# Kernel optimization log

Hardware: AMD Instinct MI355X
Metric: run time of the kernel (lower is better)

The kernel has to match this reference:

```python
import jax, jax.numpy as jnp
import numpy as np

B, F, V, E, D1, DD, L2 = 4096, 32, 50000, 64, 256, 16, 128


def setup_inputs() -> dict:
    key = jax.random.key(0)
    ks = jax.random.split(key, 16)
    s = 0.05  # small init scale to keep tanh unsaturated
    return {
        "sparse": jax.random.randint(ks[0], (B, F), 0, V, dtype=jnp.int32),
        "dense": jax.random.normal(ks[1], (B, DD), dtype=jnp.float32),
        "tables": jax.random.normal(ks[2], (F, V, E), dtype=jnp.float32) * s,
        "Wz": jax.random.normal(ks[3], (D1, F, E), dtype=jnp.float32) * s,
        "bz": jnp.zeros((D1,), jnp.float32),
        "Wpi": jax.random.normal(ks[4], (D1, F, F), dtype=jnp.float32) * s,
        "bpi": jnp.zeros((D1,), jnp.float32),
        "Wpo": jax.random.normal(ks[5], (D1, E, E), dtype=jnp.float32) * s,
        "bpo": jnp.zeros((D1,), jnp.float32),
        "B1": jax.random.normal(ks[6], (D1,), dtype=jnp.float32) * s,
        "W1": jax.random.normal(ks[7], (D1 + DD, D1), dtype=jnp.float32) * s,
        "b1": jnp.zeros((D1,), jnp.float32),
        "W2": jax.random.normal(ks[8], (D1, L2), dtype=jnp.float32) * s,
        "b2": jnp.zeros((L2,), jnp.float32),
        "W3": jax.random.normal(ks[9], (L2, 1), dtype=jnp.float32) * s,
        "b3": jnp.zeros((1,), jnp.float32),
    }


def reference(sparse, dense, tables, Wz, bz, Wpi, bpi, Wpo, bpo, B1,
              W1, b1, W2, b2, W3, b3):
    # Embedding lookup: per-field table gather -> [B, F, E]
    emb = tables[jnp.arange(F)[None, :], sparse]
    # Lz: Conv1d(in=F, kernel=E) over [B, F, E] == full contraction -> [B, D1]
    Lz = jnp.einsum('bfe,dfe->bd', emb, Wz) + bz
    # Inner product: [B, F, F], then Conv1d(in=F, kernel=F) full contraction
    inner = jnp.einsum('bie,bje->bij', emb, emb)
    Lp_inner = jnp.einsum('bij,dij->bd', inner, Wpi) + bpi
    # Outer product: sum_{i,j} x_i^T x_j == s^T s with s = sum_i x_i (exact rewrite)
    s = emb.sum(axis=1)                      # [B, E]
    outer = s[:, :, None] * s[:, None, :]    # [B, E, E]
    Lp_outer = jnp.einsum('bij,dij->bd', outer, Wpo) + bpo
    L1 = Lz + Lp_inner + Lp_outer + B1       # [B, D1]
    deep_x = jnp.concatenate([L1, dense], axis=1)  # [B, D1+DD]
    h = jnp.tanh(deep_x @ W1 + b1)
    h = jnp.tanh(h @ W2 + b2)
    out = (h @ W3 + b3)[:, 0]                # [B]
    return out
```

## Files before the change

kernel.cpp:

```cpp
#include <hip/hip_runtime.h>
#include <hip/hip_bf16.h>

#define B_    4096
#define F_    32
#define V_    50000
#define E_    64
#define D1_   256
#define DD_   16
#define L2N_  128
#define KX    3072
#define KTOT  7168
#define NKC   8

typedef __bf16 bf16x8 __attribute__((ext_vector_type(8)));
typedef float  f32x4  __attribute__((ext_vector_type(4)));

typedef __attribute__((address_space(1))) const void gvoid;
typedef __attribute__((address_space(3))) void svoid;

__device__ __forceinline__ ushort f2b(float f){
  __bf16 h = (__bf16)f; return __builtin_bit_cast(ushort, h);
}
__device__ __forceinline__ float b2f(ushort u){
  return __uint_as_float(((uint)u) << 16);
}
__device__ __forceinline__ float blo(uint u){ return __uint_as_float(u << 16); }
__device__ __forceinline__ float bhi(uint u){ return __uint_as_float(u & 0xffff0000u); }
__device__ __forceinline__ void gload16(const void* g, void* l){
  __builtin_amdgcn_global_load_lds((gvoid*)g, (svoid*)l, 16, 0, 0);
}

__global__ __launch_bounds__(256) void prep_gather(
    const float* __restrict__ Wz, const float* __restrict__ Wpi,
    const float* __restrict__ Wpo, const float* __restrict__ W1,
    const float* __restrict__ W2,
    const int* __restrict__ sparse, const float* __restrict__ tables,
    ushort* __restrict__ WBb, ushort* __restrict__ W1b, ushort* __restrict__ W2b,
    ushort* __restrict__ Xb, ushort* __restrict__ Sb) {
  __shared__ ushort gsh[4][32 * 72];
  int bid = blockIdx.x, t = threadIdx.x;
  if (bid < 640) {
    if (bid < 256) {
      int n = bid;
#pragma unroll
      for (int j = 0; j < 7; ++j) {
        int k4 = (j * 256 + t) * 4;
        float4 v;
        if (k4 < 2048)      v = *(const float4*)&Wz [(size_t)n * 2048 + k4];
        else if (k4 < 3072) v = *(const float4*)&Wpi[(size_t)n * 1024 + (k4 - 2048)];
        else                v = *(const float4*)&Wpo[(size_t)n * 4096 + (k4 - 3072)];
        ushort4 o = make_ushort4(f2b(v.x), f2b(v.y), f2b(v.z), f2b(v.w));
        *(ushort4*)&WBb[(size_t)n * KTOT + k4] = o;
      }
    } else if (bid < 512) {
      int n = bid - 256;
      float v0 = (t < 272) ? W1[(size_t)t * 256 + n] : 0.f;
      W1b[(size_t)n * 288 + t] = f2b(v0);
      if (t < 32) {
        int k2 = 256 + t;
        float v1 = (k2 < 272) ? W1[(size_t)k2 * 256 + n] : 0.f;
        W1b[(size_t)n * 288 + k2] = f2b(v1);
      }
    } else {
      int n = bid - 512;
      W2b[(size_t)n * 256 + t] = f2b(W2[(size_t)t * 128 + n]);
    }
    return;
  }

  int w = t >> 6, l = t & 63;
  int b = (bid - 640) * 4 + w;
  int fr = l & 15, q = l >> 4;

  int i0 = sparse[b * F_ + fr];
  int i1 = sparse[b * F_ + 16 + fr];
  const float* r0 = tables + ((size_t)fr * V_ + i0) * 64;
  const float* r1 = tables + ((size_t)(16 + fr) * V_ + i1) * 64;

  float4 v[2][2][2];
#pragma unroll
  for (int ks = 0; ks < 2; ++ks) {
    v[0][ks][0] = *(const float4*)(r0 + ks * 32 + q * 8);
    v[0][ks][1] = *(const float4*)(r0 + ks * 32 + q * 8 + 4);
    v[1][ks][0] = *(const float4*)(r1 + ks * 32 + q * 8);
    v[1][ks][1] = *(const float4*)(r1 + ks * 32 + q * 8 + 4);
  }

  bf16x8 fg[2][2];
#pragma unroll
  for (int rh = 0; rh < 2; ++rh)
#pragma unroll
    for (int ks = 0; ks < 2; ++ks) {
      bf16x8 a;
      a[0] = (__bf16)v[rh][ks][0].x; a[1] = (__bf16)v[rh][ks][0].y;
      a[2] = (__bf16)v[rh][ks][0].z; a[3] = (__bf16)v[rh][ks][0].w;
      a[4] = (__bf16)v[rh][ks][1].x; a[5] = (__bf16)v[rh][ks][1].y;
      a[6] = (__bf16)v[rh][ks][1].z; a[7] = (__bf16)v[rh][ks][1].w;
      fg[rh][ks] = a;
      *(bf16x8*)&Xb[(size_t)b * KX + (rh * 16 + fr) * 64 + ks * 32 + q * 8] = a;
    }

  float sv[2][8];
#pragma unroll
  for (int ks = 0; ks < 2; ++ks) {
    sv[ks][0] = v[0][ks][0].x + v[1][ks][0].x; sv[ks][1] = v[0][ks][0].y + v[1][ks][0].y;
    sv[ks][2] = v[0][ks][0].z + v[1][ks][0].z; sv[ks][3] = v[0][ks][0].w + v[1][ks][0].w;
    sv[ks][4] = v[0][ks][1].x + v[1][ks][1].x; sv[ks][5] = v[0][ks][1].y + v[1][ks][1].y;
    sv[ks][6] = v[0][ks][1].z + v[1][ks][1].z; sv[ks][7] = v[0][ks][1].w + v[1][ks][1].w;
  }
#pragma unroll
  for (int m = 1; m < 16; m <<= 1)
#pragma unroll
    for (int ks = 0; ks < 2; ++ks)
#pragma unroll
      for (int j = 0; j < 8; ++j)
        sv[ks][j] += __shfl_xor(sv[ks][j], m, 64);
  if (fr == 0) {
#pragma unroll
    for (int ks = 0; ks < 2; ++ks) {
      ushort4 o0 = make_ushort4(f2b(sv[ks][0]), f2b(sv[ks][1]), f2b(sv[ks][2]), f2b(sv[ks][3]));
      ushort4 o1 = make_ushort4(f2b(sv[ks][4]), f2b(sv[ks][5]), f2b(sv[ks][6]), f2b(sv[ks][7]));
      *(ushort4*)&Sb[(size_t)b * 64 + ks * 32 + q * 8]     = o0;
      *(ushort4*)&Sb[(size_t)b * 64 + ks * 32 + q * 8 + 4] = o1;
    }
  }

  f32x4 g[2][2] = {};
#pragma unroll
  for (int ks = 0; ks < 2; ++ks)
#pragma unroll
    for (int ri = 0; ri < 2; ++ri)
#pragma unroll
      for (int rj = 0; rj < 2; ++rj)
        g[ri][rj] = __builtin_amdgcn_mfma_f32_16x16x32_bf16(
            fg[ri][ks], fg[rj][ks], g[ri][rj], 0, 0, 0);

#pragma unroll
  for (int ri = 0; ri < 2; ++ri)
#pragma unroll
    for (int rj = 0; rj < 2; ++rj)
#pragma unroll
      for (int r = 0; r < 4; ++r)
        gsh[w][(ri * 16 + q * 4 + r) * 72 + rj * 16 + fr] = f2b(g[ri][rj][r]);
  {
    int rrow = l >> 1, rcol = (l & 1) * 16;
    uint4 ga = *(const uint4*)&gsh[w][rrow * 72 + rcol];
    uint4 gb = *(const uint4*)&gsh[w][rrow * 72 + rcol + 8];
    size_t dst = (size_t)b * KX + 2048 + rrow * 32 + rcol;
    *(uint4*)&Xb[dst]     = ga;
    *(uint4*)&Xb[dst + 8] = gb;
  }
}

__global__ __launch_bounds__(512, 1) void gemm_l1(
    const ushort* __restrict__ Xb, const ushort* __restrict__ WBb,
    const ushort* __restrict__ Sb, ushort* __restrict__ Lp) {
  __shared__ __align__(16) ushort As[2][128 * 64];
  __shared__ __align__(16) ushort Bs[2][256 * 64];
  __shared__ ushort Ssl[128 * 18];

  int bid = blockIdx.x;
  int kc  = bid & 7;
  int mT  = bid >> 3;
  int bRow = mT * 128;
  int kt0 = kc * 14;
  int i_start = min(max(0, kt0 - 48), 48);

  int tid = threadIdx.x, w = tid >> 6, l = tid & 63;
  int wm = (w >> 2) * 64, wn = (w & 3) * 64;
  int fr = l & 15, q = l >> 4;

#pragma unroll
  for (int r = 0; r < 2; ++r) {
    int p = r * 1024 + tid * 2;
    int row = p >> 4, col = p & 15;
    *(ushort2*)&Ssl[row * 18 + col] =
        *(const ushort2*)&Sb[(size_t)(bRow + row) * 64 + i_start + col];
  }

  uint4 sregu[4][2];
#pragma unroll
  for (int mi = 0; mi < 4; ++mi) {
    int grow = bRow + wm + mi * 16 + fr;
    sregu[mi][0] = *(const uint4*)&Sb[(size_t)grow * 64 + q * 8];
    sregu[mi][1] = *(const uint4*)&Sb[(size_t)grow * 64 + 32 + q * 8];
  }

  int r8 = l >> 3;
  int sg = ((l & 7) ^ r8) * 8;

  auto stageA = [&](int bI, int kt) {
    const ushort* src = Xb + (size_t)(bRow + w * 16 + r8) * KX + kt * 64 + sg;
#pragma unroll
    for (int c = 0; c < 2; ++c)
      gload16(src + (size_t)(c * 8) * KX, &As[bI][(w * 16 + c * 8) * 64]);
  };
  auto stageB = [&](int bI, int kt) {
    const ushort* src = WBb + (size_t)(w * 32 + r8) * KTOT + kt * 64 + sg;
#pragma unroll
    for (int c = 0; c < 4; ++c)
      gload16(src + (size_t)(c * 8) * KTOT, &Bs[bI][(w * 32 + c * 8) * 64]);
  };

  f32x4 acc[4][4] = {};
  bf16x8 af[4][2], bfr[4][2];
  int buf = 0;

  if (kt0 < 48) stageA(0, kt0);
  stageB(0, kt0);
  __syncthreads();

#pragma unroll
  for (int tl = 0; tl < 14; ++tl) {
    int kt = kt0 + tl;
    if (tl + 1 < 14) {
      if (kt + 1 < 48) stageA(buf ^ 1, kt + 1);
      stageB(buf ^ 1, kt + 1);
    }

#pragma unroll
    for (int ni = 0; ni < 4; ++ni) {
      int col = wn + ni * 16 + fr;
#pragma unroll
      for (int ks = 0; ks < 2; ++ks) {
        int slot = (ks * 4 + q) ^ (col & 7);
        bfr[ni][ks] = *(const bf16x8*)&Bs[buf][col * 64 + slot * 8];
      }
    }
    if (kt < 48) {
#pragma unroll
      for (int mi = 0; mi < 4; ++mi) {
        int row = wm + mi * 16 + fr;
#pragma unroll
        for (int ks = 0; ks < 2; ++ks) {
          int slot = (ks * 4 + q) ^ (row & 7);
          af[mi][ks] = *(const bf16x8*)&As[buf][row * 64 + slot * 8];
        }
      }
    } else {
      int iloc = kt - 48 - i_start;
#pragma unroll
      for (int mi = 0; mi < 4; ++mi) {
        float si = b2f(Ssl[(wm + mi * 16 + fr) * 18 + iloc]);
#pragma unroll
        for (int ks = 0; ks < 2; ++ks) {
          uint4 uv = sregu[mi][ks];
          bf16x8 a;
          a[0] = (__bf16)(si * blo(uv.x)); a[1] = (__bf16)(si * bhi(uv.x));
          a[2] = (__bf16)(si * blo(uv.y)); a[3] = (__bf16)(si * bhi(uv.y));
          a[4] = (__bf16)(si * blo(uv.z)); a[5] = (__bf16)(si * bhi(uv.z));
          a[6] = (__bf16)(si * blo(uv.w)); a[7] = (__bf16)(si * bhi(uv.w));
          af[mi][ks] = a;
        }
      }
    }
#pragma unroll
    for (int ks = 0; ks < 2; ++ks)
#pragma unroll
      for (int mi = 0; mi < 4; ++mi)
#pragma unroll
        for (int ni = 0; ni < 4; ++ni)
          acc[mi][ni] = __builtin_amdgcn_mfma_f32_16x16x32_bf16(
              af[mi][ks], bfr[ni][ks], acc[mi][ni], 0, 0, 0);
    __syncthreads();
    buf ^= 1;
  }

  ushort* Lpk = Lp + (size_t)kc * (B_ * D1_);
#pragma unroll
  for (int mi = 0; mi < 4; ++mi) {
    int row0 = bRow + wm + mi * 16 + q * 4;
#pragma unroll
    for (int ni = 0; ni < 4; ++ni) {
      int col = wn + ni * 16 + fr;
#pragma unroll
      for (int r = 0; r < 4; ++r)
        Lpk[(size_t)(row0 + r) * D1_ + col] = f2b(acc[mi][ni][r]);
    }
  }
}

__global__ __launch_bounds__(256) void mlp_fused(
    const ushort* __restrict__ Lp, const float* __restrict__ dense,
    const ushort* __restrict__ W1b, const ushort* __restrict__ W2b,
    const float* __restrict__ bz, const float* __restrict__ bpi,
    const float* __restrict__ bpo, const float* __restrict__ B1v,
    const float* __restrict__ b1, const float* __restrict__ b2,
    const float* __restrict__ W3, const float* __restrict__ b3,
    float* __restrict__ out) {
  __shared__ ushort hs[16 * 264];
  __shared__ ushort h2s[16 * 136];
  __shared__ float bvs[256];
  int b0 = blockIdx.x * 16;
  int tid = threadIdx.x, w = tid >> 6, l = tid & 63;
  int row = l & 15, q = l >> 4;
  int wn = w * 64;

  bvs[tid] = bz[tid] + bpi[tid] + bpo[tid] + B1v[tid];
  __syncthreads();

  f32x4 acc1[4] = {};
  for (int kt = 0; kt < 9; ++kt) {
    int k0 = kt * 32 + q * 8;
    bf16x8 afr;
    if (kt < 8) {
      size_t base = (size_t)(b0 + row) * D1_ + k0;
      float s[8] = {0.f, 0.f, 0.f, 0.f, 0.f, 0.f, 0.f, 0.f};
#pragma unroll
      for (int p = 0; p < NKC; ++p) {
        uint4 u = *(const uint4*)&Lp[(size_t)p * (B_ * D1_) + base];
        s[0] += blo(u.x); s[1] += bhi(u.x);
        s[2] += blo(u.y); s[3] += bhi(u.y);
        s[4] += blo(u.z); s[5] += bhi(u.z);
        s[6] += blo(u.w); s[7] += bhi(u.w);
      }
      float4 bv0 = *(const float4*)&bvs[k0];
      float4 bv1 = *(const float4*)&bvs[k0 + 4];
      afr[0] = (__bf16)(s[0] + bv0.x); afr[1] = (__bf16)(s[1] + bv0.y);
      afr[2] = (__bf16)(s[2] + bv0.z); afr[3] = (__bf16)(s[3] + bv0.w);
      afr[4] = (__bf16)(s[4] + bv1.x); afr[5] = (__bf16)(s[5] + bv1.y);
      afr[6] = (__bf16)(s[6] + bv1.z); afr[7] = (__bf16)(s[7] + bv1.w);
    } else if (q < 2) {
      float4 u0 = *(const float4*)&dense[(size_t)(b0 + row) * DD_ + q * 8];
      float4 u1 = *(const float4*)&dense[(size_t)(b0 + row) * DD_ + q * 8 + 4];
      afr[0] = (__bf16)u0.x; afr[1] = (__bf16)u0.y; afr[2] = (__bf16)u0.z; afr[3] = (__bf16)u0.w;
      afr[4] = (__bf16)u1.x; afr[5] = (__bf16)u1.y; afr[6] = (__bf16)u1.z; afr[7] = (__bf16)u1.w;
    } else {
      afr = (bf16x8)(__bf16)0.f;
    }
#pragma unroll
    for (int ni = 0; ni < 4; ++ni) {
      bf16x8 bfr = *(const bf16x8*)&W1b[(size_t)(wn + ni * 16 + row) * 288 + k0];
      acc1[ni] = __builtin_amdgcn_mfma_f32_16x16x32_bf16(afr, bfr, acc1[ni], 0, 0, 0);
    }
  }
#pragma unroll
  for (int ni = 0; ni < 4; ++ni) {
    int col = wn + ni * 16 + row;
    float bias = b1[col];
#pragma unroll
    for (int r = 0; r < 4; ++r)
      hs[(q * 4 + r) * 264 + col] = f2b(tanhf(acc1[ni][r] + bias));
  }
  __syncthreads();

  int wn2 = w * 32;
  f32x4 acc2[2] = {};
  for (int kt = 0; kt < 8; ++kt) {
    int k0 = kt * 32 + q * 8;
    bf16x8 afr = *(const bf16x8*)&hs[row * 264 + k0];
#pragma unroll
    for (int ni = 0; ni < 2; ++ni) {
      bf16x8 bfr = *(const bf16x8*)&W2b[(size_t)(wn2 + ni * 16 + row) * 256 + k0];
      acc2[ni] = __builtin_amdgcn_mfma_f32_16x16x32_bf16(afr, bfr, acc2[ni], 0, 0, 0);
    }
  }
#pragma unroll
  for (int ni = 0; ni < 2; ++ni) {
    int col = wn2 + ni * 16 + row;
    float bias = b2[col];
#pragma unroll
    for (int r = 0; r < 4; ++r)
      h2s[(q * 4 + r) * 136 + col] = f2b(tanhf(acc2[ni][r] + bias));
  }
  __syncthreads();

  if (w == 0) {
    int rr = l >> 2, g = l & 3;
    float sum = 0.f;
#pragma unroll
    for (int jj = 0; jj < 32; ++jj) {
      int j = g * 32 + jj;
      sum += b2f(h2s[rr * 136 + j]) * W3[j];
    }
    sum += __shfl_xor(sum, 1, 64);
    sum += __shfl_xor(sum, 2, 64);
    if (g == 0) out[b0 + rr] = sum + b3[0];
  }
}

extern "C" void kernel_launch(void* const* d_in, const int* in_sizes, int n_in,
                              void* d_out, int out_size, void* d_ws, size_t ws_size,
                              hipStream_t stream) {
  const int*   sparse = (const int*)  d_in[0];
  const float* dense  = (const float*)d_in[1];
  const float* tables = (const float*)d_in[2];
  const float* Wz     = (const float*)d_in[3];
  const float* bz     = (const float*)d_in[4];
  const float* Wpi    = (const float*)d_in[5];
  const float* bpi    = (const float*)d_in[6];
  const float* Wpo    = (const float*)d_in[7];
  const float* bpo    = (const float*)d_in[8];
  const float* B1v    = (const float*)d_in[9];
  const float* W1     = (const float*)d_in[10];
  const float* b1     = (const float*)d_in[11];
  const float* W2     = (const float*)d_in[12];
  const float* b2     = (const float*)d_in[13];
  const float* W3     = (const float*)d_in[14];
  const float* b3     = (const float*)d_in[15];
  float* out = (float*)d_out;

  char* ws = (char*)d_ws;
  ushort* Xb  = (ushort*)(ws);
  ushort* WBb = (ushort*)(ws + 25165824);
  ushort* W1b = (ushort*)(ws + 28835840);
  ushort* W2b = (ushort*)(ws + 28983296);
  ushort* Sb  = (ushort*)(ws + 29048832);
  ushort* Lp  = (ushort*)(ws + 29573120);

  prep_gather<<<dim3(1664), dim3(256), 0, stream>>>(
      Wz, Wpi, Wpo, W1, W2, sparse, tables, WBb, W1b, W2b, Xb, Sb);
  gemm_l1    <<<dim3(256),  dim3(512), 0, stream>>>(Xb, WBb, Sb, Lp);
  mlp_fused  <<<dim3(256),  dim3(256), 0, stream>>>(
      Lp, dense, W1b, W2b, bz, bpi, bpo, B1v, b1, b2, W3, b3, out);
}
```

Measured before the change: 59.77 us.

## Fuse prep, GEMM and MLP into one cooperative kernel with grid syncs

Merges the three kernel launches (weight prep plus gather, split-K layer-1 GEMM, fused MLP) into a single cooperative kernel of 256 blocks of 512 threads. The phases are separated by grid.sync and share one static shared-memory buffer. The aim is to remove launch gaps and inter-kernel drain and fill. The gather and MLP phases are remapped to 256 large blocks, with each wave handling two samples sequentially and fewer, wider workgroups in the MLP. That lowers parallelism and latency hiding in the gather phase, and the grid barriers add their own cost.

```diff
diff --git a/kernel.cpp b/kernel.cpp
--- a/kernel.cpp
+++ b/kernel.cpp
@@ -1,5 +1,7 @@
 #include <hip/hip_runtime.h>
 #include <hip/hip_bf16.h>
+#include <hip/hip_cooperative_groups.h>
+namespace cg = cooperative_groups;
 
 #define B_    4096
 #define F_    32
@@ -30,352 +32,354 @@
   __builtin_amdgcn_global_load_lds((gvoid*)g, (svoid*)l, 16, 0, 0);
 }
 
-__global__ __launch_bounds__(256) void prep_gather(
-    const float* __restrict__ Wz, const float* __restrict__ Wpi,
-    const float* __restrict__ Wpo, const float* __restrict__ W1,
-    const float* __restrict__ W2,
-    const int* __restrict__ sparse, const float* __restrict__ tables,
-    ushort* __restrict__ WBb, ushort* __restrict__ W1b, ushort* __restrict__ W2b,
-    ushort* __restrict__ Xb, ushort* __restrict__ Sb) {
-  __shared__ ushort gsh[4][32 * 72];
-  int bid = blockIdx.x, t = threadIdx.x;
-  if (bid < 640) {
-    if (bid < 256) {
+__global__ __launch_bounds__(512) void fused_all(
+    const int* __restrict__ sparse, const float* __restrict__ dense,
+    const float* __restrict__ tables,
+    const float* __restrict__ Wz, const float* __restrict__ bz,
+    const float* __restrict__ Wpi, const float* __restrict__ bpi,
+    const float* __restrict__ Wpo, const float* __restrict__ bpo,
+    const float* __restrict__ B1v, const float* __restrict__ W1,
+    const float* __restrict__ b1, const float* __restrict__ W2,
+    const float* __restrict__ b2, const float* __restrict__ W3,
+    const float* __restrict__ b3, float* __restrict__ out,
+    char* __restrict__ ws) {
+  __shared__ __align__(16) ushort smem[51456];
+  cg::grid_group grid = cg::this_grid();
+
+  ushort* Xb  = (ushort*)(ws);
+  ushort* WBb = (ushort*)(ws + 25165824);
+  ushort* W1b = (ushort*)(ws + 28835840);
+  ushort* W2b = (ushort*)(ws + 28983296);
+  ushort* Sb  = (ushort*)(ws + 29048832);
+  ushort* Lp  = (ushort*)(ws + 29573120);
+
+  int bid = blockIdx.x, tid = threadIdx.x;
+  int w = tid >> 6, l = tid & 63;
+  int fr = l & 15, q = l >> 4;
+
+  {
+    {
       int n = bid;
 #pragma unroll
-      for (int j = 0; j < 7; ++j) {
-        int k4 = (j * 256 + t) * 4;
-        float4 v;
-        if (k4 < 2048)      v = *(const float4*)&Wz [(size_t)n * 2048 + k4];
-        else if (k4 < 3072) v = *(const float4*)&Wpi[(size_t)n * 1024 + (k4 - 2048)];
-        else                v = *(const float4*)&Wpo[(size_t)n * 4096 + (k4 - 3072)];
-        ushort4 o = make_ushort4(f2b(v.x), f2b(v.y), f2b(v.z), f2b(v.w));
-        *(ushort4*)&WBb[(size_t)n * KTOT + k4] = o;
-      }
-    } else if (bid < 512) {
-      int n = bid - 256;
-      float v0 = (t < 272) ? W1[(size_t)t * 256 + n] : 0.f;
-      W1b[(size_t)n * 288 + t] = f2b(v0);
-      if (t < 32) {
-        int k2 = 256 + t;
-        float v1 = (k2 < 272) ? W1[(size_t)k2 * 256 + n] : 0.f;
-        W1b[(size_t)n * 288 + k2] = f2b(v1);
-      }
-    } else {
-      int n = bid - 512;
-      W2b[(size_t)n * 256 + t] = f2b(W2[(size_t)t * 128 + n]);
-    }
-    return;
+      for (int j = 0; j < 4; ++j) {
+        int k4 = (j * 512 + tid) * 4;
+        if (k4 < KTOT) {
+          float4 v;
+          if (k4 < 2048)      v = *(const float4*)&Wz [(size_t)n * 2048 + k4];
+          else if (k4 < 3072) v = *(const float4*)&Wpi[(size_t)n * 1024 + (k4 - 2048)];
+          else                v = *(const float4*)&Wpo[(size_t)n * 4096 + (k4 - 3072)];
+          *(ushort4*)&WBb[(size_t)n * KTOT + k4] =
+              make_ushort4(f2b(v.x), f2b(v.y), f2b(v.z), f2b(v.w));
+        }
+      }
+      if (tid < 288) {
+        float v0 = (tid < 272) ? W1[(size_t)tid * 256 + n] : 0.f;
+        W1b[(size_t)n * 288 + tid] = f2b(v0);
+      }
+      if (n < 128 && tid < 256)
+        W2b[(size_t)n * 256 + tid] = f2b(W2[(size_t)tid * 128 + n]);
+    }
+
+    ushort* gsh = smem + w * (32 * 72);
+    for (int ss = 0; ss < 2; ++ss) {
+      int b = bid * 16 + w * 2 + ss;
+
+      int i0 = sparse[b * F_ + fr];
+      int i1 = sparse[b * F_ + 16 + fr];
+      const float* r0 = tables + ((size_t)fr * V_ + i0) * 64;
+      const float* r1 = tables + ((size_t)(16 + fr) * V_ + i1) * 64;
+
+      float4 v[2][2][2];
+#pragma unroll
+      for (int ks = 0; ks < 2; ++ks) {
+        v[0][ks][0] = *(const float4*)(r0 + ks * 32 + q * 8);
+        v[0][ks][1] = *(const float4*)(r0 + ks * 32 + q * 8 + 4);
+        v[1][ks][0] = *(const float4*)(r1 + ks * 32 + q * 8);
+        v[1][ks][1] = *(const float4*)(r1 + ks * 32 + q * 8 + 4);
+      }
+
+      bf16x8 fg[2][2];
+#pragma unroll
+      for (int rh = 0; rh < 2; ++rh)
+#pragma unroll
+        for (int ks = 0; ks < 2; ++ks) {
+          bf16x8 a;
+          a[0] = (__bf16)v[rh][ks][0].x; a[1] = (__bf16)v[rh][ks][0].y;
+          a[2] = (__bf16)v[rh][ks][0].z; a[3] = (__bf16)v[rh][ks][0].w;
+          a[4] = (__bf16)v[rh][ks][1].x; a[5] = (__bf16)v[rh][ks][1].y;
+          a[6] = (__bf16)v[rh][ks][1].z; a[7] = (__bf16)v[rh][ks][1].w;
+          fg[rh][ks] = a;
+          *(bf16x8*)&Xb[(size_t)b * KX + (rh * 16 + fr) * 64 + ks * 32 + q * 8] = a;
+        }
+
+      float sv[2][8];
+#pragma unroll
+      for (int ks = 0; ks < 2; ++ks) {
+        sv[ks][0] = v[0][ks][0].x + v[1][ks][0].x; sv[ks][1] = v[0][ks][0].y + v[1][ks][0].y;
+        sv[ks][2] = v[0][ks][0].z + v[1][ks][0].z; sv[ks][3] = v[0][ks][0].w + v[1][ks][0].w;
+        sv[ks][4] = v[0][ks][1].x + v[1][ks][1].x; sv[ks][5] = v[0][ks][1].y + v[1][ks][1].y;
+        sv[ks][6] = v[0][ks][1].z + v[1][ks][1].z; sv[ks][7] = v[0][ks][1].w + v[1][ks][1].w;
+      }
+#pragma unroll
+      for (int m = 1; m < 16; m <<= 1)
+#pragma unroll
+        for (int ks = 0; ks < 2; ++ks)
+#pragma unroll
+          for (int j = 0; j < 8; ++j)
+            sv[ks][j] += __shfl_xor(sv[ks][j], m, 64);
+      if (fr == 0) {
+#pragma unroll
+        for (int ks = 0; ks < 2; ++ks) {
+          ushort4 o0 = make_ushort4(f2b(sv[ks][0]), f2b(sv[ks][1]), f2b(sv[ks][2]), f2b(sv[ks][3]));
+          ushort4 o1 = make_ushort4(f2b(sv[ks][4]), f2b(sv[ks][5]), f2b(sv[ks][6]), f2b(sv[ks][7]));
+          *(ushort4*)&Sb[(size_t)b * 64 + ks * 32 + q * 8]     = o0;
+          *(ushort4*)&Sb[(size_t)b * 64 + ks * 32 + q * 8 + 4] = o1;
+        }
+      }
+
+      f32x4 g[2][2] = {};
+#pragma unroll
+      for (int ks = 0; ks < 2; ++ks)
+#pragma unroll
+        for (int ri = 0; ri < 2; ++ri)
+#pragma unroll
+          for (int rj = 0; rj < 2; ++rj)
+            g[ri][rj] = __builtin_amdgcn_mfma_f32_16x16x32_bf16(
+                fg[ri][ks], fg[rj][ks], g[ri][rj], 0, 0, 0);
+
+#pragma unroll
+      for (int ri = 0; ri < 2; ++ri)
+#pragma unroll
+        for (int rj = 0; rj < 2; ++rj)
+#pragma unroll
+          for (int r = 0; r < 4; ++r)
+            gsh[(ri * 16 + q * 4 + r) * 72 + rj * 16 + fr] = f2b(g[ri][rj][r]);
+      {
+        int rrow = l >> 1, rcol = (l & 1) * 16;
+        uint4 ga = *(const uint4*)&gsh[rrow * 72 + rcol];
+        uint4 gb = *(const uint4*)&gsh[rrow * 72 + rcol + 8];
+        size_t dst = (size_t)b * KX + 2048 + rrow * 32 + rcol;
+        *(uint4*)&Xb[dst]     = ga;
+        *(uint4*)&Xb[dst + 8] = gb;
+      }
+    }
   }
-
-  int w = t >> 6, l = t & 63;
-  int b = (bid - 640) * 4 + w;
-  int fr = l & 15, q = l >> 4;
-
-  int i0 = sparse[b * F_ + fr];
-  int i1 = sparse[b * F_ + 16 + fr];
-  const float* r0 = tables + ((size_t)fr * V_ + i0) * 64;
-  const float* r1 = tables + ((size_t)(16 + fr) * V_ + i1) * 64;
-
-  float4 v[2][2][2];
-#pragma unroll
-  for (int ks = 0; ks < 2; ++ks) {
-    v[0][ks][0] = *(const float4*)(r0 + ks * 32 + q * 8);
-    v[0][ks][1] = *(const float4*)(r0 + ks * 32 + q * 8 + 4);
-    v[1][ks][0] = *(const float4*)(r1 + ks * 32 + q * 8);
-    v[1][ks][1] = *(const float4*)(r1 + ks * 32 + q * 8 + 4);
+  grid.sync();
+
+  {
+    ushort* As0 = smem;
+    ushort* As1 = As0 + 128 * 64;
+    ushort* Bs0 = As1 + 128 * 64;
+    ushort* Bs1 = Bs0 + 256 * 64;
+    ushort* Ssl = Bs1 + 256 * 64;
+
+    int kc  = bid & 7;
+    int mT  = bid >> 3;
+    int bRow = mT * 128;
+    int kt0 = kc * 14;
+    int i_start = min(max(0, kt0 - 48), 48);
+
+    int wm = (w >> 2) * 64, wn = (w & 3) * 64;
+
+#pragma unroll
+    for (int r = 0; r < 2; ++r) {
+      int p = r * 1024 + tid * 2;
+      int row = p >> 4, col = p & 15;
+      *(ushort2*)&Ssl[row * 18 + col] =
+          *(const ushort2*)&Sb[(size_t)(bRow + row) * 64 + i_start + col];
+    }
+
+    uint4 sregu[4][2];
+#pragma unroll
+    for (int mi = 0; mi < 4; ++mi) {
+      int grow = bRow + wm + mi * 16 + fr;
+      sregu[mi][0] = *(const uint4*)&Sb[(size_t)grow * 64 + q * 8];
+      sregu[mi][1] = *(const uint4*)&Sb[(size_t)grow * 64 + 32 + q * 8];
+    }
+
+    int r8 = l >> 3;
+    int sg = ((l & 7) ^ r8) * 8;
+
+    auto stageA = [&](ushort* dst, int kt) {
+      const ushort* src = Xb + (size_t)(bRow + w * 16 + r8) * KX + kt * 64 + sg;
+#pragma unroll
+      for (int c = 0; c < 2; ++c)
+        gload16(src + (size_t)(c * 8) * KX, &dst[(w * 16 + c * 8) * 64]);
+    };
+    auto stageB = [&](ushort* dst, int kt) {
+      const ushort* src = WBb + (size_t)(w * 32 + r8) * KTOT + kt * 64 + sg;
+#pragma unroll
+      for (int c = 0; c < 4; ++c)
+        gload16(src + (size_t)(c * 8) * KTOT, &dst[(w * 32 + c * 8) * 64]);
+    };
+
+    f32x4 acc[4][4] = {};
+    bf16x8 af[4][2], bfr[4][2];
+
+    if (kt0 < 48) stageA(As0, kt0);
+    stageB(Bs0, kt0);
+    __syncthreads();
+
+#pragma unroll
+    for (int tl = 0; tl < 14; ++tl) {
+      int kt = kt0 + tl;
+      ushort* Ac = (tl & 1) ? As1 : As0;
+      ushort* Bc = (tl & 1) ? Bs1 : Bs0;
+      ushort* An = (tl & 1) ? As0 : As1;
+      ushort* Bn = (tl & 1) ? Bs0 : Bs1;
+      if (tl + 1 < 14) {
+        if (kt + 1 < 48) stageA(An, kt + 1);
+        stageB(Bn, kt + 1);
+      }
+
+#pragma unroll
+      for (int ni = 0; ni < 4; ++ni) {
+        int col = wn + ni * 16 + fr;
+#pragma unroll
+        for (int ks = 0; ks < 2; ++ks) {
+          int slot = (ks * 4 + q) ^ (col & 7);
+          bfr[ni][ks] = *(const bf16x8*)&Bc[col * 64 + slot * 8];
+        }
+      }
+      if (kt < 48) {
+#pragma unroll
+        for (int mi = 0; mi < 4; ++mi) {
+          int row = wm + mi * 16 + fr;
+#pragma unroll
+          for (int ks = 0; ks < 2; ++ks) {
+            int slot = (ks * 4 + q) ^ (row & 7);
+            af[mi][ks] = *(const bf16x8*)&Ac[row * 64 + slot * 8];
+          }
+        }
+      } else {
+        int iloc = kt - 48 - i_start;
+#pragma unroll
+        for (int mi = 0; mi < 4; ++mi) {
+          float si = b2f(Ssl[(wm + mi * 16 + fr) * 18 + iloc]);
+#pragma unroll
+          for (int ks = 0; ks < 2; ++ks) {
+            uint4 uv = sregu[mi][ks];
+            bf16x8 a;
+            a[0] = (__bf16)(si * blo(uv.x)); a[1] = (__bf16)(si * bhi(uv.x));
+            a[2] = (__bf16)(si * blo(uv.y)); a[3] = (__bf16)(si * bhi(uv.y));
+            a[4] = (__bf16)(si * blo(uv.z)); a[5] = (__bf16)(si * bhi(uv.z));
+            a[6] = (__bf16)(si * blo(uv.w)); a[7] = (__bf16)(si * bhi(uv.w));
+            af[mi][ks] = a;
+          }
+        }
+      }
+#pragma unroll
+      for (int ks = 0; ks < 2; ++ks)
+#pragma unroll
+        for (int mi = 0; mi < 4; ++mi)
+#pragma unroll
+          for (int ni = 0; ni < 4; ++ni)
+            acc[mi][ni] = __builtin_amdgcn_mfma_f32_16x16x32_bf16(
+                af[mi][ks], bfr[ni][ks], acc[mi][ni], 0, 0, 0);
+      __syncthreads();
+    }
+
+    ushort* Lpk = Lp + (size_t)kc * (B_ * D1_);
+#pragma unroll
+    for (int mi = 0; mi < 4; ++mi) {
+      int row0 = bRow + wm + mi * 16 + q * 4;
+#pragma unroll
+      for (int ni = 0; ni < 4; ++ni) {
+        int col = wn + ni * 16 + fr;
+#pragma unroll
+        for (int r = 0; r < 4; ++r)
+          Lpk[(size_t)(row0 + r) * D1_ + col] = f2b(acc[mi][ni][r]);
+      }
+    }
   }
-
-  bf16x8 fg[2][2];
-#pragma unroll
-  for (int rh = 0; rh < 2; ++rh)
-#pragma unroll
-    for (int ks = 0; ks < 2; ++ks) {
-      bf16x8 a;
-      a[0] = (__bf16)v[rh][ks][0].x; a[1] = (__bf16)v[rh][ks][0].y;
-      a[2] = (__bf16)v[rh][ks][0].z; a[3] = (__bf16)v[rh][ks][0].w;
-      a[4] = (__bf16)v[rh][ks][1].x; a[5] = (__bf16)v[rh][ks][1].y;
-      a[6] = (__bf16)v[rh][ks][1].z; a[7] = (__bf16)v[rh][ks][1].w;
-      fg[rh][ks] = a;
-      *(bf16x8*)&Xb[(size_t)b * KX + (rh * 16 + fr) * 64 + ks * 32 + q * 8] = a;
-    }
-
-  float sv[2][8];
-#pragma unroll
-  for (int ks = 0; ks < 2; ++ks) {
-    sv[ks][0] = v[0][ks][0].x + v[1][ks][0].x; sv[ks][1] = v[0][ks][0].y + v[1][ks][0].y;
-    sv[ks][2] = v[0][ks][0].z + v[1][ks][0].z; sv[ks][3] = v[0][ks][0].w + v[1][ks][0].w;
-    sv[ks][4] = v[0][ks][1].x + v[1][ks][1].x; sv[ks][5] = v[0][ks][1].y + v[1][ks][1].y;
-    sv[ks][6] = v[0][ks][1].z + v[1][ks][1].z; sv[ks][7] = v[0][ks][1].w + v[1][ks][1].w;
-  }
-#pragma unroll
-  for (int m = 1; m < 16; m <<= 1)
-#pragma unroll
-    for (int ks = 0; ks < 2; ++ks)
-#pragma unroll
-      for (int j = 0; j < 8; ++j)
-        sv[ks][j] += __shfl_xor(sv[ks][j], m, 64);
-  if (fr == 0) {
-#pragma unroll
-    for (int ks = 0; ks < 2; ++ks) {
-      ushort4 o0 = make_ushort4(f2b(sv[ks][0]), f2b(sv[ks][1]), f2b(sv[ks][2]), f2b(sv[ks][3]));
-      ushort4 o1 = make_ushort4(f2b(sv[ks][4]), f2b(sv[ks][5]), f2b(sv[ks][6]), f2b(sv[ks][7]));
-      *(ushort4*)&Sb[(size_t)b * 64 + ks * 32 + q * 8]     = o0;
-      *(ushort4*)&Sb[(size_t)b * 64 + ks * 32 + q * 8 + 4] = o1;
-    }
-  }
-
-  f32x4 g[2][2] = {};
-#pragma unroll
-  for (int ks = 0; ks < 2; ++ks)
-#pragma unroll
-    for (int ri = 0; ri < 2; ++ri)
-#pragma unroll
-      for (int rj = 0; rj < 2; ++rj)
-        g[ri][rj] = __builtin_amdgcn_mfma_f32_16x16x32_bf16(
-            fg[ri][ks], fg[rj][ks], g[ri][rj], 0, 0, 0);
-
-#pragma unroll
-  for (int ri = 0; ri < 2; ++ri)
-#pragma unroll
-    for (int rj = 0; rj < 2; ++rj)
+  grid.sync();
+
+  {
+    ushort* hs  = smem;
+    ushort* h2s = smem + 16 * 264;
+    float*  bvs = (float*)(smem + 16 * 264 + 16 * 136);
+
+    int b0 = bid * 16;
+    int row = fr;
+
+    if (tid < 256) bvs[tid] = bz[tid] + bpi[tid] + bpo[tid] + B1v[tid];
+    __syncthreads();
+
+    int wn = w * 32;
+    f32x4 acc1[2] = {};
+    for (int kt = 0; kt < 9; ++kt) {
+      int k0 = kt * 32 + q * 8;
+      bf16x8 afr;
+      if (kt < 8) {
+        size_t base = (size_t)(b0 + row) * D1_ + k0;
+        float s[8] = {0.f, 0.f, 0.f, 0.f, 0.f, 0.f, 0.f, 0.f};
+#pragma unroll
+        for (int p = 0; p < NKC; ++p) {
+          uint4 u = *(const uint4*)&Lp[(size_t)p * (B_ * D1_) + base];
+          s[0] += blo(u.x); s[1] += bhi(u.x);
+          s[2] += blo(u.y); s[3] += bhi(u.y);
+          s[4] += blo(u.z); s[5] += bhi(u.z);
+          s[6] += blo(u.w); s[7] += bhi(u.w);
+        }
+        float4 bv0 = *(const float4*)&bvs[k0];
+        float4 bv1 = *(const float4*)&bvs[k0 + 4];
+        afr[0] = (__bf16)(s[0] + bv0.x); afr[1] = (__bf16)(s[1] + bv0.y);
+        afr[2] = (__bf16)(s[2] + bv0.z); afr[3] = (__bf16)(s[3] + bv0.w);
+        afr[4] = (__bf16)(s[4] + bv1.x); afr[5] = (__bf16)(s[5] + bv1.y);
+        afr[6] = (__bf16)(s[6] + bv1.z); afr[7] = (__bf16)(s[7] + bv1.w);
+      } else if (q < 2) {
+        float4 u0 = *(const float4*)&dense[(size_t)(b0 + row) * DD_ + q * 8];
+        float4 u1 = *(const float4*)&dense[(size_t)(b0 + row) * DD_ + q * 8 + 4];
+        afr[0] = (__bf16)u0.x; afr[1] = (__bf16)u0.y; afr[2] = (__bf16)u0.z; afr[3] = (__bf16)u0.w;
+        afr[4] = (__bf16)u1.x; afr[5] = (__bf16)u1.y; afr[6] = (__bf16)u1.z; afr[7] = (__bf16)u1.w;
+      } else {
+        afr = (bf16x8)(__bf16)0.f;
+      }
+#pragma unroll
+      for (int ni = 0; ni < 2; ++ni) {
+        bf16x8 bfr = *(const bf16x8*)&W1b[(size_t)(wn + ni * 16 + row) * 288 + k0];
+        acc1[ni] = __builtin_amdgcn_mfma_f32_16x16x32_bf16(afr, bfr, acc1[ni], 0, 0, 0);
+      }
+    }
+#pragma unroll
+    for (int ni = 0; ni < 2; ++ni) {
+      int col = wn + ni * 16 + row;
+      float bias = b1[col];
 #pragma unroll
       for (int r = 0; r < 4; ++r)
-        gsh[w][(ri * 16 + q * 4 + r) * 72 + rj * 16 + fr] = f2b(g[ri][rj][r]);
-  {
-    int rrow = l >> 1, rcol = (l & 1) * 16;
-    uint4 ga = *(const uint4*)&gsh[w][rrow * 72 + rcol];
-    uint4 gb = *(const uint4*)&gsh[w][rrow * 72 + rcol + 8];
-    size_t dst = (size_t)b * KX + 2048 + rrow * 32 + rcol;
-    *(uint4*)&Xb[dst]     = ga;
-    *(uint4*)&Xb[dst + 8] = gb;
-  }
-}
-
-__global__ __launch_bounds__(512, 1) void gemm_l1(
-    const ushort* __restrict__ Xb, const ushort* __restrict__ WBb,
-    const ushort* __restrict__ Sb, ushort* __restrict__ Lp) {
-  __shared__ __align__(16) ushort As[2][128 * 64];
-  __shared__ __align__(16) ushort Bs[2][256 * 64];
-  __shared__ ushort Ssl[128 * 18];
-
-  int bid = blockIdx.x;
-  int kc  = bid & 7;
-  int mT  = bid >> 3;
-  int bRow = mT * 128;
-  int kt0 = kc * 14;
-  int i_start = min(max(0, kt0 - 48), 48);
-
-  int tid = threadIdx.x, w = tid >> 6, l = tid & 63;
-  int wm = (w >> 2) * 64, wn = (w & 3) * 64;
-  int fr = l & 15, q = l >> 4;
-
-#pragma unroll
-  for (int r = 0; r < 2; ++r) {
-    int p = r * 1024 + tid * 2;
-    int row = p >> 4, col = p & 15;
-    *(ushort2*)&Ssl[row * 18 + col] =
-        *(const ushort2*)&Sb[(size_t)(bRow + row) * 64 + i_start + col];
-  }
-
-  uint4 sregu[4][2];
-#pragma unroll
-  for (int mi = 0; mi < 4; ++mi) {
-    int grow = bRow + wm + mi * 16 + fr;
-    sregu[mi][0] = *(const uint4*)&Sb[(size_t)grow * 64 + q * 8];
-    sregu[mi][1] = *(const uint4*)&Sb[(size_t)grow * 64 + 32 + q * 8];
-  }
-
-  int r8 = l >> 3;
-  int sg = ((l & 7) ^ r8) * 8;
-
-  auto stageA = [&](int bI, int kt) {
-    const ushort* src = Xb + (size_t)(bRow + w * 16 + r8) * KX + kt * 64 + sg;
-#pragma unroll
-    for (int c = 0; c < 2; ++c)
-      gload16(src + (size_t)(c * 8) * KX, &As[bI][(w * 16 + c * 8) * 64]);
-  };
-  auto stageB = [&](int bI, int kt) {
-    const ushort* src = WBb + (size_t)(w * 32 + r8) * KTOT + kt * 64 + sg;
-#pragma unroll
-    for (int c = 0; c < 4; ++c)
-      gload16(src + (size_t)(c * 8) * KTOT, &Bs[bI][(w * 32 + c * 8) * 64]);
-  };
-
-  f32x4 acc[4][4] = {};
-  bf16x8 af[4][2], bfr[4][2];
-  int buf = 0;
-
-  if (kt0 < 48) stageA(0, kt0);
-  stageB(0, kt0);
-  __syncthreads();
-
-#pragma unroll
-  for (int tl = 0; tl < 14; ++tl) {
-    int kt = kt0 + tl;
-    if (tl + 1 < 14) {
-      if (kt + 1 < 48) stageA(buf ^ 1, kt + 1);
-      stageB(buf ^ 1, kt + 1);
-    }
-
-#pragma unroll
-    for (int ni = 0; ni < 4; ++ni) {
-      int col = wn + ni * 16 + fr;
-#pragma unroll
-      for (int ks = 0; ks < 2; ++ks) {
-        int slot = (ks * 4 + q) ^ (col & 7);
-        bfr[ni][ks] = *(const bf16x8*)&Bs[buf][col * 64 + slot * 8];
-      }
-    }
-    if (kt < 48) {
-#pragma unroll
-      for (int mi = 0; mi < 4; ++mi) {
-        int row = wm + mi * 16 + fr;
-#pragma unroll
-        for (int ks = 0; ks < 2; ++ks) {
-          int slot = (ks * 4 + q) ^ (row & 7);
-          af[mi][ks] = *(const bf16x8*)&As[buf][row * 64 + slot * 8];
-        }
-      }
-    } else {
-      int iloc = kt - 48 - i_start;
-#pragma unroll
-      for (int mi = 0; mi < 4; ++mi) {
-        float si = b2f(Ssl[(wm + mi * 16 + fr) * 18 + iloc]);
-#pragma unroll
-        for (int ks = 0; ks < 2; ++ks) {
-          uint4 uv = sregu[mi][ks];
-          bf16x8 a;
-          a[0] = (__bf16)(si * blo(uv.x)); a[1] = (__bf16)(si * bhi(uv.x));
-          a[2] = (__bf16)(si * blo(uv.y)); a[3] = (__bf16)(si * bhi(uv.y));
-          a[4] = (__bf16)(si * blo(uv.z)); a[5] = (__bf16)(si * bhi(uv.z));
-          a[6] = (__bf16)(si * blo(uv.w)); a[7] = (__bf16)(si * bhi(uv.w));
-          af[mi][ks] = a;
-        }
-      }
-    }
-#pragma unroll
-    for (int ks = 0; ks < 2; ++ks)
-#pragma unroll
-      for (int mi = 0; mi < 4; ++mi)
-#pragma unroll
-        for (int ni = 0; ni < 4; ++ni)
-          acc[mi][ni] = __builtin_amdgcn_mfma_f32_16x16x32_bf16(
-              af[mi][ks], bfr[ni][ks], acc[mi][ni], 0, 0, 0);
+        hs[(q * 4 + r) * 264 + col] = f2b(tanhf(acc1[ni][r] + bias));
+    }
     __syncthreads();
-    buf ^= 1;
-  }
-
-  ushort* Lpk = Lp + (size_t)kc * (B_ * D1_);
-#pragma unroll
-  for (int mi = 0; mi < 4; ++mi) {
-    int row0 = bRow + wm + mi * 16 + q * 4;
-#pragma unroll
-    for (int ni = 0; ni < 4; ++ni) {
-      int col = wn + ni * 16 + fr;
+
+    int wn2 = w * 16;
+    f32x4 acc2 = {};
+    for (int kt = 0; kt < 8; ++kt) {
+      int k0 = kt * 32 + q * 8;
+      bf16x8 afr = *(const bf16x8*)&hs[row * 264 + k0];
+      bf16x8 bfr = *(const bf16x8*)&W2b[(size_t)(wn2 + row) * 256 + k0];
+      acc2 = __builtin_amdgcn_mfma_f32_16x16x32_bf16(afr, bfr, acc2, 0, 0, 0);
+    }
+    {
+      int col = wn2 + row;
+      float bias = b2[col];
 #pragma unroll
       for (int r = 0; r < 4; ++r)
-        Lpk[(size_t)(row0 + r) * D1_ + col] = f2b(acc[mi][ni][r]);
-    }
-  }
-}
-
-__global__ __launch_bounds__(256) void mlp_fused(
-    const ushort* __restrict__ Lp, const float* __restrict__ dense,
-    const ushort* __restrict__ W1b, const ushort* __restrict__ W2b,
-    const float* __restrict__ bz, const float* __restrict__ bpi,
-    const float* __restrict__ bpo, const float* __restrict__ B1v,
-    const float* __restrict__ b1, const float* __restrict__ b2,
-    const float* __restrict__ W3, const float* __restrict__ b3,
-    float* __restrict__ out) {
-  __shared__ ushort hs[16 * 264];
-  __shared__ ushort h2s[16 * 136];
-  __shared__ float bvs[256];
-  int b0 = blockIdx.x * 16;
-  int tid = threadIdx.x, w = tid >> 6, l = tid & 63;
-  int row = l & 15, q = l >> 4;
-  int wn = w * 64;
-
-  bvs[tid] = bz[tid] + bpi[tid] + bpo[tid] + B1v[tid];
-  __syncthreads();
-
-  f32x4 acc1[4] = {};
-  for (int kt = 0; kt < 9; ++kt) {
-    int k0 = kt * 32 + q * 8;
-    bf16x8 afr;
-    if (kt < 8) {
-      size_t base = (size_t)(b0 + row) * D1_ + k0;
-      float s[8] = {0.f, 0.f, 0.f, 0.f, 0.f, 0.f, 0.f, 0.f};
-#pragma unroll
-      for (int p = 0; p < NKC; ++p) {
-        uint4 u = *(const uint4*)&Lp[(size_t)p * (B_ * D1_) + base];
-        s[0] += blo(u.x); s[1] += bhi(u.x);
-        s[2] += blo(u.y); s[3] += bhi(u.y);
-        s[4] += blo(u.z); s[5] += bhi(u.z);
-        s[6] += blo(u.w); s[7] += bhi(u.w);
-      }
-      float4 bv0 = *(const float4*)&bvs[k0];
-      float4 bv1 = *(const float4*)&bvs[k0 + 4];
-      afr[0] = (__bf16)(s[0] + bv0.x); afr[1] = (__bf16)(s[1] + bv0.y);
-      afr[2] = (__bf16)(s[2] + bv0.z); afr[3] = (__bf16)(s[3] + bv0.w);
-      afr[4] = (__bf16)(s[4] + bv1.x); afr[5] = (__bf16)(s[5] + bv1.y);
-      afr[6] = (__bf16)(s[6] + bv1.z); afr[7] = (__bf16)(s[7] + bv1.w);
-    } else if (q < 2) {
-      float4 u0 = *(const float4*)&dense[(size_t)(b0 + row) * DD_ + q * 8];
-      float4 u1 = *(const float4*)&dense[(size_t)(b0 + row) * DD_ + q * 8 + 4];
-      afr[0] = (__bf16)u0.x; afr[1] = (__bf16)u0.y; afr[2] = (__bf16)u0.z; afr[3] = (__bf16)u0.w;
-      afr[4] = (__bf16)u1.x; afr[5] = (__bf16)u1.y; afr[6] = (__bf16)u1.z; afr[7] = (__bf16)u1.w;
-    } else {
-      afr = (bf16x8)(__bf16)0.f;
-    }
-#pragma unroll
-    for (int ni = 0; ni < 4; ++ni) {
-      bf16x8 bfr = *(const bf16x8*)&W1b[(size_t)(wn + ni * 16 + row) * 288 + k0];
-      acc1[ni] = __builtin_amdgcn_mfma_f32_16x16x32_bf16(afr, bfr, acc1[ni], 0, 0, 0);
-    }
-  }
-#pragma unroll
-  for (int ni = 0; ni < 4; ++ni) {
-    int col = wn + ni * 16 + row;
-    float bias = b1[col];
-#pragma unroll
-    for (int r = 0; r < 4; ++r)
-      hs[(q * 4 + r) * 264 + col] = f2b(tanhf(acc1[ni][r] + bias));
-  }
-  __syncthreads();
-
-  int wn2 = w * 32;
-  f32x4 acc2[2] = {};
-  for (int kt = 0; kt < 8; ++kt) {
-    int k0 = kt * 32 + q * 8;
-    bf16x8 afr = *(const bf16x8*)&hs[row * 264 + k0];
-#pragma unroll
-    for (int ni = 0; ni < 2; ++ni) {
-      bf16x8 bfr = *(const bf16x8*)&W2b[(size_t)(wn2 + ni * 16 + row) * 256 + k0];
-      acc2[ni] = __builtin_amdgcn_mfma_f32_16x16x32_bf16(afr, bfr, acc2[ni], 0, 0, 0);
-    }
-  }
-#pragma unroll
-  for (int ni = 0; ni < 2; ++ni) {
-    int col = wn2 + ni * 16 + row;
-    float bias = b2[col];
-#pragma unroll
-    for (int r = 0; r < 4; ++r)
-      h2s[(q * 4 + r) * 136 + col] = f2b(tanhf(acc2[ni][r] + bias));
-  }
-  __syncthreads();
-
-  if (w == 0) {
-    int rr = l >> 2, g = l & 3;
-    float sum = 0.f;
-#pragma unroll
-    for (int jj = 0; jj < 32; ++jj) {
-      int j = g * 32 + jj;
-      sum += b2f(h2s[rr * 136 + j]) * W3[j];
-    }
-    sum += __shfl_xor(sum, 1, 64);
-    sum += __shfl_xor(sum, 2, 64);
-    if (g == 0) out[b0 + rr] = sum + b3[0];
+        h2s[(q * 4 + r) * 136 + col] = f2b(tanhf(acc2[r] + bias));
+    }
+    __syncthreads();
+
+    if (w == 0) {
+      int rr = l >> 2, g = l & 3;
+      float sum = 0.f;
+#pragma unroll
+      for (int jj = 0; jj < 32; ++jj) {
+        int j = g * 32 + jj;
+        sum += b2f(h2s[rr * 136 + j]) * W3[j];
+      }
+      sum += __shfl_xor(sum, 1, 64);
+      sum += __shfl_xor(sum, 2, 64);
+      if (g == 0) out[b0 + rr] = sum + b3[0];
+    }
   }
 }
 
@@ -399,18 +403,15 @@
   const float* W3     = (const float*)d_in[14];
   const float* b3     = (const float*)d_in[15];
   float* out = (float*)d_out;
-
   char* ws = (char*)d_ws;
-  ushort* Xb  = (ushort*)(ws);
-  ushort* WBb = (ushort*)(ws + 25165824);
-  ushort* W1b = (ushort*)(ws + 28835840);
-  ushort* W2b = (ushort*)(ws + 28983296);
-  ushort* Sb  = (ushort*)(ws + 29048832);
-  ushort* Lp  = (ushort*)(ws + 29573120);
-
-  prep_gather<<<dim3(1664), dim3(256), 0, stream>>>(
-      Wz, Wpi, Wpo, W1, W2, sparse, tables, WBb, W1b, W2b, Xb, Sb);
-  gemm_l1    <<<dim3(256),  dim3(512), 0, stream>>>(Xb, WBb, Sb, Lp);
-  mlp_fused  <<<dim3(256),  dim3(256), 0, stream>>>(
-      Lp, dense, W1b, W2b, bz, bpi, bpo, B1v, b1, b2, W3, b3, out);
+
+  void* kargs[] = {
+    (void*)&sparse, (void*)&dense, (void*)&tables,
+    (void*)&Wz, (void*)&bz, (void*)&Wpi, (void*)&bpi,
+    (void*)&Wpo, (void*)&bpo, (void*)&B1v, (void*)&W1,
+    (void*)&b1, (void*)&W2, (void*)&b2, (void*)&W3,
+    (void*)&b3, (void*)&out, (void*)&ws
+  };
+  hipLaunchCooperativeKernel((const void*)fused_all, dim3(256), dim3(512),
+                             kargs, 0, stream);
 }
```

Result: slower. 147.9 us (+147.5%).
